# Kernel tuning notes

Hardware: AMD Instinct MI355X
Metric: run time of the kernel (lower is better)

## Reference

```python
import jax, jax.numpy as jnp
import numpy as np

BATCH = 2
L = 2048
D_MODEL = 1024
D_STATE = 16
D_CONV = 4
EXPAND = 2
D_INNER = EXPAND * D_MODEL  # 2048
DT_RANK = (D_MODEL + 15) // 16  # 64


def setup_inputs() -> dict:
    key = jax.random.key(0)
    ks = jax.random.split(key, 12)
    f = jnp.float32
    hidden_states = jax.random.normal(ks[0], (BATCH, L, D_MODEL), f)
    input2 = jax.random.normal(ks[1], (BATCH, L, D_MODEL), f)
    in_proj1_w = jax.random.normal(ks[2], (D_INNER, D_MODEL), f) * (D_MODEL ** -0.5)
    in_proj2_w = jax.random.normal(ks[3], (D_INNER, D_MODEL), f) * (D_MODEL ** -0.5)
    conv_w = jax.random.normal(ks[4], (D_INNER, 1, D_CONV), f) * (D_CONV ** -0.5)
    conv_b = jax.random.normal(ks[5], (D_INNER,), f) * 0.02
    x_proj_w = jax.random.normal(ks[6], (DT_RANK + 2 * D_STATE, D_INNER), f) * (D_INNER ** -0.5)
    dt_std = DT_RANK ** -0.5
    dt_proj_w = jax.random.uniform(ks[7], (D_INNER, DT_RANK), f, -dt_std, dt_std)
    # dt bias init: inverse softplus of log-uniform dt in [1e-3, 1e-1]
    dt = jnp.exp(jax.random.uniform(ks[8], (D_INNER,), f) * (np.log(0.1) - np.log(0.001)) + np.log(0.001))
    dt = jnp.clip(dt, 1e-4, None)
    dt_proj_b = dt + jnp.log(-jnp.expm1(-dt))
    # A_log init: log(1..d_state) broadcast over channels
    A_log = jnp.log(jnp.broadcast_to(jnp.arange(1, D_STATE + 1, dtype=f), (D_INNER, D_STATE)))
    D = jnp.ones((D_INNER,), f)
    out_proj_w = jax.random.normal(ks[9], (D_MODEL, D_INNER), f) * (D_INNER ** -0.5)
    return dict(hidden_states=hidden_states, input2=input2, in_proj1_w=in_proj1_w,
                in_proj2_w=in_proj2_w, conv_w=conv_w, conv_b=conv_b, x_proj_w=x_proj_w,
                dt_proj_w=dt_proj_w, dt_proj_b=dt_proj_b, A_log=A_log, D=D,
                out_proj_w=out_proj_w)


def _forward(hidden_states, input2, in_proj1_w, in_proj2_w, conv_w, conv_b,
             x_proj_w, dt_proj_w, dt_proj_b, A_log, D, out_proj_w):
    # in_proj: (B,L,Dm) -> (B,d_inner,L)
    x = jnp.einsum('bld,ed->bel', hidden_states, in_proj1_w)
    z = jnp.einsum('bld,ed->bel', input2, in_proj2_w)
    # causal depthwise conv1d (left pad d_conv-1, equiv to torch pad+truncate) + SiLU
    xc = jax.lax.conv_general_dilated(x, conv_w, (1,), [(D_CONV - 1, 0)],
                                      dimension_numbers=('NCH', 'OIH', 'NCH'),
                                      feature_group_count=D_INNER)
    x = jax.nn.silu(xc + conv_b[None, :, None])
    # x_proj -> dt, B, C
    x_dbl = jnp.einsum('bel,re->brl', x, x_proj_w)  # (B, dt_rank+2n, L)
    dt = x_dbl[:, :DT_RANK]
    Bm = x_dbl[:, DT_RANK:DT_RANK + D_STATE]       # (B, n, L)
    Cm = x_dbl[:, DT_RANK + D_STATE:]               # (B, n, L)
    delta = jnp.einsum('brl,er->bel', dt, dt_proj_w)
    delta = jax.nn.softplus(delta + dt_proj_b[None, :, None])  # (B, d_inner, L)
    A = -jnp.exp(A_log)  # (d_inner, n)
    # selective scan over time (time-major for lax.scan)
    dlt = jnp.transpose(delta, (2, 0, 1))  # (L, B, d)
    u = jnp.transpose(x, (2, 0, 1))        # (L, B, d)
    Bt = jnp.transpose(Bm, (2, 0, 1))      # (L, B, n)
    Ct = jnp.transpose(Cm, (2, 0, 1))      # (L, B, n)

    def step(state, inp):
        d_t, u_t, B_t, C_t = inp
        dA = jnp.exp(d_t[..., None] * A)                        # (B, d, n)
        state = state * dA + (d_t * u_t)[..., None] * B_t[:, None, :]
        y_t = jnp.einsum('bdn,bn->bd', state, C_t)
        return state, y_t

    init = jnp.zeros((hidden_states.shape[0], D_INNER, D_STATE), x.dtype)
    _, ys = jax.lax.scan(step, init, (dlt, u, Bt, Ct))
    y = jnp.transpose(ys, (1, 2, 0)) + D[None, :, None] * x  # (B, d, L)
    y = y * jax.nn.silu(z)
    out = jnp.einsum('bel,de->bld', y, out_proj_w)  # out_proj, no bias
    return out


def reference(hidden_states, input2, in_proj1_w, in_proj2_w, conv_w, conv_b,
              x_proj_w, dt_proj_w, dt_proj_b, A_log, D, out_proj_w):
    return _forward(hidden_states, input2, in_proj1_w, in_proj2_w, conv_w, conv_b,
                    x_proj_w, dt_proj_w, dt_proj_b, A_log, D, out_proj_w)
```

## Files before the change

kernel.cpp:

```cpp
#include <hip/hip_runtime.h>
#include <cstddef>
#include <cmath>
#include <type_traits>

#define BATCH 2
#define LSEQ 2048
#define DM 1024
#define DSTATE 16
#define DI 2048
#define DTR 64
#define XDR 96
#define NC 64
#define TC 32
#define PN (4096 * 96)

using f32x4 = __attribute__((ext_vector_type(4))) float;
using bf16x8 = __attribute__((ext_vector_type(8))) short;

__device__ __forceinline__ unsigned short f2bf(float f) {
  union { float f; unsigned int u; } c; c.f = f;
  unsigned int u = c.u;
  return (unsigned short)((u + 0x7FFFu + ((u >> 16) & 1u)) >> 16);
}
__device__ __forceinline__ float bf2f(unsigned short h) {
  union { unsigned int u; float f; } c; c.u = ((unsigned int)h) << 16;
  return c.f;
}
__device__ __forceinline__ unsigned int pack2(float a, float b) {
  return (unsigned int)f2bf(a) | ((unsigned int)f2bf(b) << 16);
}

__device__ __forceinline__ void gl_lds16(const void* g, void* l) {
  __builtin_amdgcn_global_load_lds(
      (const __attribute__((address_space(1))) void*)g,
      (__attribute__((address_space(3))) void*)l, 16, 0, 0);
}

__device__ __forceinline__ float softplus_fast(float x) {
  float ex = __expf(x);
  return (x > 20.f) ? x : __logf(1.f + ex);
}

__device__ __forceinline__ void pow_tree(float q1, float* dA) {
  float q2 = q1 * q1;
  float q3 = q2 * q1;
  float q4 = q2 * q2;
  float q8 = q4 * q4;
  float q5 = q4 * q1, q6 = q4 * q2, q7 = q4 * q3;
  dA[0] = q1;  dA[1] = q2;  dA[2] = q3;  dA[3] = q4;
  dA[4] = q5;  dA[5] = q6;  dA[6] = q7;  dA[7] = q8;
  dA[8] = q8 * q1;  dA[9] = q8 * q2;  dA[10] = q8 * q3;  dA[11] = q8 * q4;
  dA[12] = q8 * q5; dA[13] = q8 * q6; dA[14] = q8 * q7;  dA[15] = q8 * q8;
}

__global__ __launch_bounds__(256) void cvt_bf16_kernel(
    const float* __restrict__ s, unsigned short* __restrict__ d, int n8) {
  int i = blockIdx.x * 256 + threadIdx.x;
  if (i >= n8) return;
  const float4* sp = reinterpret_cast<const float4*>(s) + (size_t)i * 2;
  float4 a = sp[0], b = sp[1];
  uint4 v = make_uint4(pack2(a.x, a.y), pack2(a.z, a.w), pack2(b.x, b.y),
                       pack2(b.z, b.w));
  *(reinterpret_cast<uint4*>(d) + i) = v;
}

template <typename OutT>
__global__ __launch_bounds__(256) void gemm_bf16_t(
    const unsigned short* __restrict__ A, const unsigned short* __restrict__ B,
    OutT* __restrict__ C, int K, int lda, int ldb, int ldc) {
  __shared__ __align__(16) unsigned short As[128][64];
  __shared__ __align__(16) unsigned short Bs[128][64];

  const int tid = threadIdx.x;
  const int lane = tid & 63;
  const int w = tid >> 6;

  const int gx = gridDim.x;
  const int nwg = gx * gridDim.y;
  const int id = blockIdx.y * gx + blockIdx.x;
  const int cpx = nwg >> 3;
  const int lt = (id & 7) * cpx + (id >> 3);
  const size_t m0 = (size_t)(lt / gx) * 128;
  const size_t n0 = (size_t)(lt % gx) * 128;

  const int rsub = lane >> 3;
  const int sslot = (lane & 7) ^ rsub;
  const unsigned short* Ab = A + m0 * lda + (size_t)rsub * lda + sslot * 8;
  const unsigned short* Bb = B + n0 * ldb + (size_t)rsub * ldb + sslot * 8;

  f32x4 acc[4][4] = {};

  const int fr = lane & 15;
  const int q = lane >> 4;
  const int f7 = fr & 7;

  for (int k0 = 0; k0 < K; k0 += 64) {
#pragma unroll
    for (int i = 0; i < 4; ++i) {
      const int r0 = w * 32 + i * 8;
      gl_lds16(Ab + (size_t)r0 * lda + k0, &As[r0][0]);
      gl_lds16(Bb + (size_t)r0 * ldb + k0, &Bs[r0][0]);
    }
    __syncthreads();

    bf16x8 af[4][2], bf_[4][2];
#pragma unroll
    for (int i = 0; i < 4; ++i) {
#pragma unroll
      for (int kk = 0; kk < 2; ++kk) {
        const int sA = (((kk * 4 + q) ^ f7) << 3);
        af[i][kk] = *reinterpret_cast<const bf16x8*>(
            &As[(w >> 1) * 64 + i * 16 + fr][sA]);
        bf_[i][kk] = *reinterpret_cast<const bf16x8*>(
            &Bs[(w & 1) * 64 + i * 16 + fr][sA]);
      }
    }
#pragma unroll
    for (int kk = 0; kk < 2; ++kk)
#pragma unroll
      for (int i = 0; i < 4; ++i)
#pragma unroll
        for (int j = 0; j < 4; ++j)
          acc[i][j] = __builtin_amdgcn_mfma_f32_16x16x32_bf16(
              af[i][kk], bf_[j][kk], acc[i][j], 0, 0, 0);
    __syncthreads();
  }

  const int crb = q * 4;
#pragma unroll
  for (int i = 0; i < 4; ++i) {
    size_t row = m0 + (w >> 1) * 64 + i * 16 + crb;
#pragma unroll
    for (int j = 0; j < 4; ++j) {
      size_t col = n0 + (w & 1) * 64 + j * 16 + fr;
#pragma unroll
      for (int r = 0; r < 4; ++r) {
        if constexpr (std::is_same_v<OutT, unsigned short>)
          C[(row + r) * ldc + col] = f2bf(acc[i][j][r]);
        else
          C[(row + r) * ldc + col] = acc[i][j][r];
      }
    }
  }
}

__global__ __launch_bounds__(256) void gemm_delta(
    const unsigned short* __restrict__ A, const unsigned short* __restrict__ B,
    const float* __restrict__ bias, unsigned short* __restrict__ C, int K,
    int lda, int ldb, int ldc) {
  __shared__ __align__(16) unsigned short As[128][64];
  __shared__ __align__(16) unsigned short Bs[128][64];

  const int tid = threadIdx.x;
  const int lane = tid & 63;
  const int w = tid >> 6;

  const int gx = gridDim.x;
  const int nwg = gx * gridDim.y;
  const int id = blockIdx.y * gx + blockIdx.x;
  const int cpx = nwg >> 3;
  const int lt = (id & 7) * cpx + (id >> 3);
  const size_t m0 = (size_t)(lt / gx) * 128;
  const size_t n0 = (size_t)(lt % gx) * 128;

  const int rsub = lane >> 3;
  const int sslot = (lane & 7) ^ rsub;
  const unsigned short* Ab = A + m0 * lda + (size_t)rsub * lda + sslot * 8;
  const unsigned short* Bb = B + n0 * ldb + (size_t)rsub * ldb + sslot * 8;

  f32x4 acc[4][4] = {};

  const int fr = lane & 15;
  const int q = lane >> 4;
  const int f7 = fr & 7;

  for (int k0 = 0; k0 < K; k0 += 64) {
#pragma unroll
    for (int i = 0; i < 4; ++i) {
      const int r0 = w * 32 + i * 8;
      gl_lds16(Ab + (size_t)r0 * lda + k0, &As[r0][0]);
      gl_lds16(Bb + (size_t)r0 * ldb + k0, &Bs[r0][0]);
    }
    __syncthreads();

    bf16x8 af[4][2], bf_[4][2];
#pragma unroll
    for (int i = 0; i < 4; ++i) {
#pragma unroll
      for (int kk = 0; kk < 2; ++kk) {
        const int sA = (((kk * 4 + q) ^ f7) << 3);
        af[i][kk] = *reinterpret_cast<const bf16x8*>(
            &As[(w >> 1) * 64 + i * 16 + fr][sA]);
        bf_[i][kk] = *reinterpret_cast<const bf16x8*>(
            &Bs[(w & 1) * 64 + i * 16 + fr][sA]);
      }
    }
#pragma unroll
    for (int kk = 0; kk < 2; ++kk)
#pragma unroll
      for (int i = 0; i < 4; ++i)
#pragma unroll
        for (int j = 0; j < 4; ++j)
          acc[i][j] = __builtin_amdgcn_mfma_f32_16x16x32_bf16(
              af[i][kk], bf_[j][kk], acc[i][j], 0, 0, 0);
    __syncthreads();
  }

  const int crb = q * 4;
#pragma unroll
  for (int i = 0; i < 4; ++i) {
    size_t row = m0 + (w >> 1) * 64 + i * 16 + crb;
#pragma unroll
    for (int j = 0; j < 4; ++j) {
      size_t col = n0 + (w & 1) * 64 + j * 16 + fr;
      float bv = bias[col];
#pragma unroll
      for (int r = 0; r < 4; ++r)
        C[(row + r) * ldc + col] = f2bf(softplus_fast(acc[i][j][r] + bv));
    }
  }
}

__global__ __launch_bounds__(256) void gemm_xdbl(
    const unsigned short* __restrict__ A,
    const unsigned short* __restrict__ B,
    float* __restrict__ P) {
  __shared__ __align__(16) unsigned short As[128][64];
  __shared__ __align__(16) unsigned short Bs[96][64];

  const int tid = threadIdx.x;
  const int lane = tid & 63;
  const int w = tid >> 6;
  const size_t m0 = (size_t)blockIdx.x * 128;
  const int k0base = blockIdx.y * 512;

  const int rsub = lane >> 3;
  const int sslot = (lane & 7) ^ rsub;
  const unsigned short* Ab = A + m0 * DI + (size_t)rsub * DI + sslot * 8;
  const unsigned short* Bb = B + (size_t)rsub * DI + sslot * 8;

  f32x4 acc[4][3] = {};

  const int fr = lane & 15;
  const int q = lane >> 4;
  const int f7 = fr & 7;

  for (int ks = 0; ks < 8; ++ks) {
    const int k0 = k0base + ks * 64;
#pragma unroll
    for (int i = 0; i < 4; ++i) {
      const int r0 = w * 32 + i * 8;
      gl_lds16(Ab + (size_t)r0 * DI + k0, &As[r0][0]);
    }
#pragma unroll
    for (int i = 0; i < 3; ++i) {
      const int r0 = w * 24 + i * 8;
      gl_lds16(Bb + (size_t)r0 * DI + k0, &Bs[r0][0]);
    }
    __syncthreads();

    bf16x8 af[4][2], bf_[3][2];
#pragma unroll
    for (int kk = 0; kk < 2; ++kk) {
      const int sA = (((kk * 4 + q) ^ f7) << 3);
#pragma unroll
      for (int i = 0; i < 4; ++i)
        af[i][kk] = *reinterpret_cast<const bf16x8*>(
            &As[(w >> 1) * 64 + i * 16 + fr][sA]);
#pragma unroll
      for (int j = 0; j < 3; ++j)
        bf_[j][kk] = *reinterpret_cast<const bf16x8*>(
            &Bs[(w & 1) * 48 + j * 16 + fr][sA]);
    }
#pragma unroll
    for (int kk = 0; kk < 2; ++kk)
#pragma unroll
      for (int i = 0; i < 4; ++i)
#pragma unroll
        for (int j = 0; j < 3; ++j)
          acc[i][j] = __builtin_amdgcn_mfma_f32_16x16x32_bf16(
              af[i][kk], bf_[j][kk], acc[i][j], 0, 0, 0);
    __syncthreads();
  }

  float* Pz = P + (size_t)blockIdx.y * PN;
  const int crb = q * 4;
#pragma unroll
  for (int i = 0; i < 4; ++i) {
    size_t row = m0 + (w >> 1) * 64 + i * 16 + crb;
#pragma unroll
    for (int j = 0; j < 3; ++j) {
      int col = (w & 1) * 48 + j * 16 + fr;
#pragma unroll
      for (int r = 0; r < 4; ++r) Pz[(row + r) * XDR + col] = acc[i][j][r];
    }
  }
}

__global__ __launch_bounds__(256) void reduce4x_kernel(
    const float* __restrict__ P, unsigned short* __restrict__ dtB,
    float* __restrict__ BC) {
  int i = blockIdx.x * 256 + threadIdx.x;
  int row = i / XDR, col = i - row * XDR;
  float s = (P[i] + P[PN + i]) + (P[2 * PN + i] + P[3 * PN + i]);
  if (col < 64)
    dtB[row * 64 + col] = f2bf(s);
  else
    BC[row * 32 + (col - 64)] = s;
}

__global__ __launch_bounds__(256) void conv_silu_kernel(
    const float* __restrict__ x, const float* __restrict__ w,
    const float* __restrict__ cb, unsigned short* __restrict__ out) {
  int idx = blockIdx.x * 256 + threadIdx.x;
  int e4 = idx % (DI / 4);
  int bl = idx / (DI / 4);
  int l = bl % LSEQ;
  int e = e4 * 4;

  const float4* cw = reinterpret_cast<const float4*>(w);
  float4 w0 = cw[e], w1 = cw[e + 1], w2 = cw[e + 2], w3 = cw[e + 3];
  float4 acc = *reinterpret_cast<const float4*>(&cb[e]);

#define TAPK(K, COMP)                                                       \
  {                                                                         \
    int ls = l - 3 + (K);                                                   \
    if (ls >= 0) {                                                          \
      float4 xv = *reinterpret_cast<const float4*>(                         \
          &x[((size_t)(bl) - 3 + (K)) * DI + e]);                           \
      acc.x = fmaf(xv.x, w0.COMP, acc.x);                                   \
      acc.y = fmaf(xv.y, w1.COMP, acc.y);                                   \
      acc.z = fmaf(xv.z, w2.COMP, acc.z);                                   \
      acc.w = fmaf(xv.w, w3.COMP, acc.w);                                   \
    }                                                                       \
  }
  TAPK(0, x)
  TAPK(1, y)
  TAPK(2, z)
  TAPK(3, w)
#undef TAPK

  acc.x = acc.x / (1.f + expf(-acc.x));
  acc.y = acc.y / (1.f + expf(-acc.y));
  acc.z = acc.z / (1.f + expf(-acc.z));
  acc.w = acc.w / (1.f + expf(-acc.w));
  *reinterpret_cast<uint2*>(&out[(size_t)bl * DI + e]) =
      make_uint2(pack2(acc.x, acc.y), pack2(acc.z, acc.w));
}

__global__ __launch_bounds__(256) void scan_passA(
    const unsigned short* __restrict__ dB, const unsigned short* __restrict__ u,
    const float* __restrict__ bc, const float* __restrict__ A_log,
    float* __restrict__ sEnd, float* __restrict__ sProd) {
  int g = blockIdx.x * 256 + threadIdx.x;
  int e = g & (DI - 1);
  int c = (g >> 11) & (NC - 1);
  int b = g >> 17;

  const float nA0 = -__expf(A_log[e * DSTATE]);
  bool aok = true;
#pragma unroll
  for (int n = 1; n < DSTATE; ++n) {
    float nAn = -__expf(A_log[e * DSTATE + n]);
    aok = aok && (fabsf(nAn - (float)(n + 1) * nA0) <= 1e-4f * fabsf(nAn));
  }

  size_t off = ((size_t)b * LSEQ + c * TC) * DI + e;
  size_t boff = ((size_t)b * LSEQ + c * TC) * 32;

  float s[DSTATE], P[DSTATE];
#pragma unroll
  for (int n = 0; n < DSTATE; ++n) { s[n] = 0.f; P[n] = 1.f; }

  float d = bf2f(dB[off]);
  float ut = bf2f(u[off]);

  for (int t = 0; t < TC; ++t) {
    float d_n = 0.f, ut_n = 0.f;
    if (t + 1 < TC) {
      d_n = bf2f(dB[off + DI]);
      ut_n = bf2f(u[off + DI]);
    }

    float db = d * ut;
    float dA[DSTATE];
    if (aok) {
      pow_tree(__expf(d * nA0), dA);
    } else {
#pragma unroll
      for (int n = 0; n < DSTATE; ++n)
        dA[n] = __expf(-d * __expf(A_log[e * DSTATE + n]));
    }
    const float4* bcp = reinterpret_cast<const float4*>(&bc[boff]);
    float4 B0 = bcp[0], B1 = bcp[1], B2 = bcp[2], B3 = bcp[3];
    float Bv[DSTATE] = {B0.x, B0.y, B0.z, B0.w, B1.x, B1.y, B1.z, B1.w,
                        B2.x, B2.y, B2.z, B2.w, B3.x, B3.y, B3.z, B3.w};
#pragma unroll
    for (int n = 0; n < DSTATE; ++n) {
      s[n] = fmaf(s[n], dA[n], db * Bv[n]);
      P[n] *= dA[n];
    }
    off += DI;
    boff += 32;
    d = d_n; ut = ut_n;
  }

  size_t o = (((size_t)b * NC + c) * DI + e) * DSTATE;
  float4* se = reinterpret_cast<float4*>(&sEnd[o]);
  float4* sp = reinterpret_cast<float4*>(&sProd[o]);
  se[0] = make_float4(s[0], s[1], s[2], s[3]);
  se[1] = make_float4(s[4], s[5], s[6], s[7]);
  se[2] = make_float4(s[8], s[9], s[10], s[11]);
  se[3] = make_float4(s[12], s[13], s[14], s[15]);
  sp[0] = make_float4(P[0], P[1], P[2], P[3]);
  sp[1] = make_float4(P[4], P[5], P[6], P[7]);
  sp[2] = make_float4(P[8], P[9], P[10], P[11]);
  sp[3] = make_float4(P[12], P[13], P[14], P[15]);
}

__global__ __launch_bounds__(256) void scan_passB(
    float* __restrict__ sEnd, const float* __restrict__ sProd) {
  int g = blockIdx.x * 256 + threadIdx.x;
  int n = g & 15;
  int e = (g >> 4) & (DI - 1);
  int b = g >> 15;
  float s = 0.f;
  for (int c = 0; c < NC; ++c) {
    size_t o = (((size_t)b * NC + c) * DI + e) * DSTATE + n;
    float se = sEnd[o];
    float sp = sProd[o];
    sEnd[o] = s;
    s = fmaf(s, sp, se);
  }
}

__global__ __launch_bounds__(256) void scan_passC(
    const unsigned short* __restrict__ dB, const unsigned short* __restrict__ u,
    const unsigned short* __restrict__ z, const float* __restrict__ bc,
    const float* __restrict__ A_log, const float* __restrict__ Dv,
    const float* __restrict__ sInit, unsigned short* __restrict__ gOut) {
  int g = blockIdx.x * 256 + threadIdx.x;
  int e = g & (DI - 1);
  int c = (g >> 11) & (NC - 1);
  int b = g >> 17;

  const float nA0 = -__expf(A_log[e * DSTATE]);
  bool aok = true;
#pragma unroll
  for (int n = 1; n < DSTATE; ++n) {
    float nAn = -__expf(A_log[e * DSTATE + n]);
    aok = aok && (fabsf(nAn - (float)(n + 1) * nA0) <= 1e-4f * fabsf(nAn));
  }
  const float Dval = Dv[e];

  size_t off = ((size_t)b * LSEQ + c * TC) * DI + e;
  size_t boff = ((size_t)b * LSEQ + c * TC) * 32;

  float s[DSTATE];
  {
    size_t o = (((size_t)b * NC + c) * DI + e) * DSTATE;
    const float4* si = reinterpret_cast<const float4*>(&sInit[o]);
    float4 s0 = si[0], s1 = si[1], s2 = si[2], s3 = si[3];
    s[0] = s0.x; s[1] = s0.y; s[2] = s0.z; s[3] = s0.w;
    s[4] = s1.x; s[5] = s1.y; s[6] = s1.z; s[7] = s1.w;
    s[8] = s2.x; s[9] = s2.y; s[10] = s2.z; s[11] = s2.w;
    s[12] = s3.x; s[13] = s3.y; s[14] = s3.z; s[15] = s3.w;
  }

  float d = bf2f(dB[off]);
  float ut = bf2f(u[off]);
  float zt = bf2f(z[off]);

  for (int t = 0; t < TC; ++t) {
    float d_n = 0.f, ut_n = 0.f, zt_n = 0.f;
    if (t + 1 < TC) {
      d_n = bf2f(dB[off + DI]);
      ut_n = bf2f(u[off + DI]);
      zt_n = bf2f(z[off + DI]);
    }

    float db = d * ut;
    float dA[DSTATE];
    if (aok) {
      pow_tree(__expf(d * nA0), dA);
    } else {
#pragma unroll
      for (int n = 0; n < DSTATE; ++n)
        dA[n] = __expf(-d * __expf(A_log[e * DSTATE + n]));
    }
    const float4* bcp = reinterpret_cast<const float4*>(&bc[boff]);
    float4 B0 = bcp[0], B1 = bcp[1], B2 = bcp[2], B3 = bcp[3];
    float4 C0 = bcp[4], C1 = bcp[5], C2 = bcp[6], C3 = bcp[7];
    float Bv[DSTATE] = {B0.x, B0.y, B0.z, B0.w, B1.x, B1.y, B1.z, B1.w,
                        B2.x, B2.y, B2.z, B2.w, B3.x, B3.y, B3.z, B3.w};
    float Cv[DSTATE] = {C0.x, C0.y, C0.z, C0.w, C1.x, C1.y, C1.z, C1.w,
                        C2.x, C2.y, C2.z, C2.w, C3.x, C3.y, C3.z, C3.w};
    float y0 = 0.f, y1 = 0.f, y2 = 0.f, y3 = 0.f;
#pragma unroll
    for (int n = 0; n < 4; ++n) {
      s[n] = fmaf(s[n], dA[n], db * Bv[n]);
      y0 = fmaf(s[n], Cv[n], y0);
      s[n + 4] = fmaf(s[n + 4], dA[n + 4], db * Bv[n + 4]);
      y1 = fmaf(s[n + 4], Cv[n + 4], y1);
      s[n + 8] = fmaf(s[n + 8], dA[n + 8], db * Bv[n + 8]);
      y2 = fmaf(s[n + 8], Cv[n + 8], y2);
      s[n + 12] = fmaf(s[n + 12], dA[n + 12], db * Bv[n + 12]);
      y3 = fmaf(s[n + 12], Cv[n + 12], y3);
    }
    float y = (y0 + y1) + (y2 + y3);
    float gate = zt / (1.f + __expf(-zt));
    gOut[off] = f2bf((y + Dval * ut) * gate);

    off += DI;
    boff += 32;
    d = d_n; ut = ut_n; zt = zt_n;
  }
}

extern "C" void kernel_launch(void* const* d_in, const int* in_sizes, int n_in,
                              void* d_out, int out_size, void* d_ws,
                              size_t ws_size, hipStream_t stream) {
  const float* hs = (const float*)d_in[0];
  const float* in2 = (const float*)d_in[1];
  const float* w1 = (const float*)d_in[2];
  const float* w2 = (const float*)d_in[3];
  const float* cw = (const float*)d_in[4];
  const float* cb = (const float*)d_in[5];
  const float* xpw = (const float*)d_in[6];
  const float* dtw = (const float*)d_in[7];
  const float* dtb = (const float*)d_in[8];
  const float* alog = (const float*)d_in[9];
  const float* Dv = (const float*)d_in[10];
  const float* ow = (const float*)d_in[11];
  float* out = (float*)d_out;

  const size_t BLE = (size_t)BATCH * LSEQ * DI;
  const size_t BLM = (size_t)BATCH * LSEQ * DM;
  const size_t WN = (size_t)DI * DM;
  const size_t SC = (size_t)BATCH * NC * DI * DSTATE;

  float* W = (float*)d_ws;
  float* bufX = W;
  float* M2 = W + BLE;
  float* M3 = M2 + BLE / 2;
  float* M4 = M3 + BLE / 2;
  float* sEnd = M4 + BLE / 2;
  float* sProd = sEnd + SC;
  float* BC = sProd + SC;

  unsigned short* hsb = (unsigned short*)M2;
  unsigned short* zb = (unsigned short*)M2;
  unsigned short* in2b = (unsigned short*)M3;
  unsigned short* ub = (unsigned short*)M3;
  unsigned short* wb1 = (unsigned short*)M4;
  unsigned short* wb2 = wb1 + WN;
  float* xdblP = M4;
  unsigned short* xpwB = (unsigned short*)(M4 + 4 * PN);
  unsigned short* dtB = (unsigned short*)(M4 + 4 * PN + 98304 + 16);
  unsigned short* dtwB = (unsigned short*)(M4 + 4 * PN + 98304 + 131072 + 32);
  unsigned short* bufG = (unsigned short*)M4;
  unsigned short* dB = (unsigned short*)bufX;
  unsigned short* owb = (unsigned short*)sProd;

  const int M = BATCH * LSEQ;
  dim3 blk(256);

  cvt_bf16_kernel<<<(int)(BLM / 8 / 256), blk, 0, stream>>>(hs, hsb,
                                                            (int)(BLM / 8));
  cvt_bf16_kernel<<<(int)(BLM / 8 / 256), blk, 0, stream>>>(in2, in2b,
                                                            (int)(BLM / 8));
  cvt_bf16_kernel<<<(int)(WN / 8 / 256), blk, 0, stream>>>(w1, wb1,
                                                           (int)(WN / 8));
  cvt_bf16_kernel<<<(int)(WN / 8 / 256), blk, 0, stream>>>(w2, wb2,
                                                           (int)(WN / 8));
  gemm_bf16_t<float><<<dim3(DI / 128, M / 128), blk, 0, stream>>>(
      hsb, wb1, bufX, DM, DM, DM, DI);
  gemm_bf16_t<unsigned short><<<dim3(DI / 128, M / 128), blk, 0, stream>>>(
      in2b, wb2, zb, DM, DM, DM, DI);
  conv_silu_kernel<<<(M * (DI / 4)) / 256, blk, 0, stream>>>(bufX, cw, cb, ub);
  cvt_bf16_kernel<<<96, blk, 0, stream>>>(xpw, xpwB, XDR * DI / 8);
  cvt_bf16_kernel<<<64, blk, 0, stream>>>(dtw, dtwB, DI * DTR / 8);
  gemm_xdbl<<<dim3(M / 128, 4), blk, 0, stream>>>(ub, xpwB, xdblP);
  reduce4x_kernel<<<(M * XDR) / 256, blk, 0, stream>>>(xdblP, dtB, BC);
  gemm_delta<<<dim3(DI / 128, M / 128), blk, 0, stream>>>(
      dtB, dtwB, dtb, dB, DTR, DTR, DTR, DI);
  scan_passA<<<(BATCH * DI * NC) / 256, blk, 0, stream>>>(dB, ub, BC, alog,
                                                          sEnd, sProd);
  scan_passB<<<(BATCH * DI * DSTATE) / 256, blk, 0, stream>>>(sEnd, sProd);
  cvt_bf16_kernel<<<(int)(WN / 8 / 256), blk, 0, stream>>>(ow, owb,
                                                           (int)(WN / 8));
  scan_passC<<<(BATCH * DI * NC) / 256, blk, 0, stream>>>(
      dB, ub, zb, BC, alog, Dv, sEnd, bufG);
  gemm_bf16_t<float><<<dim3(DM / 128, M / 128), blk, 0, stream>>>(
      bufG, owb, out, DI, DI, DI, DM);
}
```

Baseline: 247.0 us.

## Store x projection in bf16, merge conversion launches, deepen scan prefetch

```diff
diff --git a/kernel.cpp b/kernel.cpp
--- a/kernel.cpp
+++ b/kernel.cpp
@@ -64,6 +64,26 @@
   *(reinterpret_cast<uint4*>(d) + i) = v;
 }
 
+__global__ __launch_bounds__(256) void cvt2_bf16_kernel(
+    const float* __restrict__ s1, unsigned short* __restrict__ d1,
+    const float* __restrict__ s2, unsigned short* __restrict__ d2, int n8) {
+  int i = blockIdx.x * 256 + threadIdx.x;
+  const float* s;
+  unsigned short* d;
+  int k;
+  if (i < n8) {
+    s = s1; d = d1; k = i;
+  } else {
+    s = s2; d = d2; k = i - n8;
+    if (k >= n8) return;
+  }
+  const float4* sp = reinterpret_cast<const float4*>(s) + (size_t)k * 2;
+  float4 a = sp[0], b = sp[1];
+  uint4 v = make_uint4(pack2(a.x, a.y), pack2(a.z, a.w), pack2(b.x, b.y),
+                       pack2(b.z, b.w));
+  *(reinterpret_cast<uint4*>(d) + k) = v;
+}
+
 template <typename OutT>
 __global__ __launch_bounds__(256) void gemm_bf16_t(
     const unsigned short* __restrict__ A, const unsigned short* __restrict__ B,
@@ -310,7 +330,7 @@
 }
 
 __global__ __launch_bounds__(256) void conv_silu_kernel(
-    const float* __restrict__ x, const float* __restrict__ w,
+    const unsigned short* __restrict__ x, const float* __restrict__ w,
     const float* __restrict__ cb, unsigned short* __restrict__ out) {
   int idx = blockIdx.x * 256 + threadIdx.x;
   int e4 = idx % (DI / 4);
@@ -326,12 +346,12 @@
   {                                                                         \
     int ls = l - 3 + (K);                                                   \
     if (ls >= 0) {                                                          \
-      float4 xv = *reinterpret_cast<const float4*>(                         \
+      uint2 xv = *reinterpret_cast<const uint2*>(                           \
           &x[((size_t)(bl) - 3 + (K)) * DI + e]);                           \
-      acc.x = fmaf(xv.x, w0.COMP, acc.x);                                   \
-      acc.y = fmaf(xv.y, w1.COMP, acc.y);                                   \
-      acc.z = fmaf(xv.z, w2.COMP, acc.z);                                   \
-      acc.w = fmaf(xv.w, w3.COMP, acc.w);                                   \
+      acc.x = fmaf(bf2f((unsigned short)(xv.x & 0xffff)), w0.COMP, acc.x);  \
+      acc.y = fmaf(bf2f((unsigned short)(xv.x >> 16)), w1.COMP, acc.y);     \
+      acc.z = fmaf(bf2f((unsigned short)(xv.y & 0xffff)), w2.COMP, acc.z);  \
+      acc.w = fmaf(bf2f((unsigned short)(xv.y >> 16)), w3.COMP, acc.w);     \
     }                                                                       \
   }
   TAPK(0, x)
@@ -365,44 +385,52 @@
     aok = aok && (fabsf(nAn - (float)(n + 1) * nA0) <= 1e-4f * fabsf(nAn));
   }
 
-  size_t off = ((size_t)b * LSEQ + c * TC) * DI + e;
-  size_t boff = ((size_t)b * LSEQ + c * TC) * 32;
+  const size_t off = ((size_t)b * LSEQ + c * TC) * DI + e;
+  const size_t boff0 = ((size_t)b * LSEQ + c * TC) * 32;
 
   float s[DSTATE], P[DSTATE];
 #pragma unroll
   for (int n = 0; n < DSTATE; ++n) { s[n] = 0.f; P[n] = 1.f; }
 
-  float d = bf2f(dB[off]);
-  float ut = bf2f(u[off]);
-
-  for (int t = 0; t < TC; ++t) {
-    float d_n = 0.f, ut_n = 0.f;
-    if (t + 1 < TC) {
-      d_n = bf2f(dB[off + DI]);
-      ut_n = bf2f(u[off + DI]);
-    }
-
-    float db = d * ut;
-    float dA[DSTATE];
-    if (aok) {
-      pow_tree(__expf(d * nA0), dA);
-    } else {
-#pragma unroll
-      for (int n = 0; n < DSTATE; ++n)
-        dA[n] = __expf(-d * __expf(A_log[e * DSTATE + n]));
-    }
-    const float4* bcp = reinterpret_cast<const float4*>(&bc[boff]);
-    float4 B0 = bcp[0], B1 = bcp[1], B2 = bcp[2], B3 = bcp[3];
-    float Bv[DSTATE] = {B0.x, B0.y, B0.z, B0.w, B1.x, B1.y, B1.z, B1.w,
-                        B2.x, B2.y, B2.z, B2.w, B3.x, B3.y, B3.z, B3.w};
-#pragma unroll
-    for (int n = 0; n < DSTATE; ++n) {
-      s[n] = fmaf(s[n], dA[n], db * Bv[n]);
-      P[n] *= dA[n];
-    }
-    off += DI;
-    boff += 32;
-    d = d_n; ut = ut_n;
+  unsigned short dq[4], uq[4];
+#pragma unroll
+  for (int j = 0; j < 4; ++j) {
+    size_t o = off + (size_t)j * DI;
+    dq[j] = dB[o];
+    uq[j] = u[o];
+  }
+
+  for (int tb = 0; tb < TC; tb += 4) {
+#pragma unroll
+    for (int j = 0; j < 4; ++j) {
+      const int t = tb + j;
+      float d = bf2f(dq[j]);
+      float ut = bf2f(uq[j]);
+      if (t + 4 < TC) {
+        size_t o = off + (size_t)(t + 4) * DI;
+        dq[j] = dB[o];
+        uq[j] = u[o];
+      }
+      float db = d * ut;
+      float dA[DSTATE];
+      if (aok) {
+        pow_tree(__expf(d * nA0), dA);
+      } else {
+#pragma unroll
+        for (int n = 0; n < DSTATE; ++n)
+          dA[n] = __expf(-d * __expf(A_log[e * DSTATE + n]));
+      }
+      const float4* bcp =
+          reinterpret_cast<const float4*>(&bc[boff0 + (size_t)t * 32]);
+      float4 B0 = bcp[0], B1 = bcp[1], B2 = bcp[2], B3 = bcp[3];
+      float Bv[DSTATE] = {B0.x, B0.y, B0.z, B0.w, B1.x, B1.y, B1.z, B1.w,
+                          B2.x, B2.y, B2.z, B2.w, B3.x, B3.y, B3.z, B3.w};
+#pragma unroll
+      for (int n = 0; n < DSTATE; ++n) {
+        s[n] = fmaf(s[n], dA[n], db * Bv[n]);
+        P[n] *= dA[n];
+      }
+    }
   }
 
   size_t o = (((size_t)b * NC + c) * DI + e) * DSTATE;
@@ -453,8 +481,8 @@
   }
   const float Dval = Dv[e];
 
-  size_t off = ((size_t)b * LSEQ + c * TC) * DI + e;
-  size_t boff = ((size_t)b * LSEQ + c * TC) * 32;
+  const size_t off = ((size_t)b * LSEQ + c * TC) * DI + e;
+  const size_t boff0 = ((size_t)b * LSEQ + c * TC) * 32;
 
   float s[DSTATE];
   {
@@ -467,53 +495,61 @@
     s[12] = s3.x; s[13] = s3.y; s[14] = s3.z; s[15] = s3.w;
   }
 
-  float d = bf2f(dB[off]);
-  float ut = bf2f(u[off]);
-  float zt = bf2f(z[off]);
-
-  for (int t = 0; t < TC; ++t) {
-    float d_n = 0.f, ut_n = 0.f, zt_n = 0.f;
-    if (t + 1 < TC) {
-      d_n = bf2f(dB[off + DI]);
-      ut_n = bf2f(u[off + DI]);
-      zt_n = bf2f(z[off + DI]);
-    }
-
-    float db = d * ut;
-    float dA[DSTATE];
-    if (aok) {
-      pow_tree(__expf(d * nA0), dA);
-    } else {
-#pragma unroll
-      for (int n = 0; n < DSTATE; ++n)
-        dA[n] = __expf(-d * __expf(A_log[e * DSTATE + n]));
-    }
-    const float4* bcp = reinterpret_cast<const float4*>(&bc[boff]);
-    float4 B0 = bcp[0], B1 = bcp[1], B2 = bcp[2], B3 = bcp[3];
-    float4 C0 = bcp[4], C1 = bcp[5], C2 = bcp[6], C3 = bcp[7];
-    float Bv[DSTATE] = {B0.x, B0.y, B0.z, B0.w, B1.x, B1.y, B1.z, B1.w,
-                        B2.x, B2.y, B2.z, B2.w, B3.x, B3.y, B3.z, B3.w};
-    float Cv[DSTATE] = {C0.x, C0.y, C0.z, C0.w, C1.x, C1.y, C1.z, C1.w,
-                        C2.x, C2.y, C2.z, C2.w, C3.x, C3.y, C3.z, C3.w};
-    float y0 = 0.f, y1 = 0.f, y2 = 0.f, y3 = 0.f;
-#pragma unroll
-    for (int n = 0; n < 4; ++n) {
-      s[n] = fmaf(s[n], dA[n], db * Bv[n]);
-      y0 = fmaf(s[n], Cv[n], y0);
-      s[n + 4] = fmaf(s[n + 4], dA[n + 4], db * Bv[n + 4]);
-      y1 = fmaf(s[n + 4], Cv[n + 4], y1);
-      s[n + 8] = fmaf(s[n + 8], dA[n + 8], db * Bv[n + 8]);
-      y2 = fmaf(s[n + 8], Cv[n + 8], y2);
-      s[n + 12] = fmaf(s[n + 12], dA[n + 12], db * Bv[n + 12]);
-      y3 = fmaf(s[n + 12], Cv[n + 12], y3);
-    }
-    float y = (y0 + y1) + (y2 + y3);
-    float gate = zt / (1.f + __expf(-zt));
-    gOut[off] = f2bf((y + Dval * ut) * gate);
-
-    off += DI;
-    boff += 32;
-    d = d_n; ut = ut_n; zt = zt_n;
+  unsigned short dq[4], uq[4], zq[4];
+#pragma unroll
+  for (int j = 0; j < 4; ++j) {
+    size_t o = off + (size_t)j * DI;
+    dq[j] = dB[o];
+    uq[j] = u[o];
+    zq[j] = z[o];
+  }
+
+  for (int tb = 0; tb < TC; tb += 4) {
+#pragma unroll
+    for (int j = 0; j < 4; ++j) {
+      const int t = tb + j;
+      float d = bf2f(dq[j]);
+      float ut = bf2f(uq[j]);
+      float zt = bf2f(zq[j]);
+      if (t + 4 < TC) {
+        size_t o = off + (size_t)(t + 4) * DI;
+        dq[j] = dB[o];
+        uq[j] = u[o];
+        zq[j] = z[o];
+      }
+      float db = d * ut;
+      float dA[DSTATE];
+      if (aok) {
+        pow_tree(__expf(d * nA0), dA);
+      } else {
+#pragma unroll
+        for (int n = 0; n < DSTATE; ++n)
+          dA[n] = __expf(-d * __expf(A_log[e * DSTATE + n]));
+      }
+      const float4* bcp =
+          reinterpret_cast<const float4*>(&bc[boff0 + (size_t)t * 32]);
+      float4 B0 = bcp[0], B1 = bcp[1], B2 = bcp[2], B3 = bcp[3];
+      float4 C0 = bcp[4], C1 = bcp[5], C2 = bcp[6], C3 = bcp[7];
+      float Bv[DSTATE] = {B0.x, B0.y, B0.z, B0.w, B1.x, B1.y, B1.z, B1.w,
+                          B2.x, B2.y, B2.z, B2.w, B3.x, B3.y, B3.z, B3.w};
+      float Cv[DSTATE] = {C0.x, C0.y, C0.z, C0.w, C1.x, C1.y, C1.z, C1.w,
+                          C2.x, C2.y, C2.z, C2.w, C3.x, C3.y, C3.z, C3.w};
+      float y0 = 0.f, y1 = 0.f, y2 = 0.f, y3 = 0.f;
+#pragma unroll
+      for (int n = 0; n < 4; ++n) {
+        s[n] = fmaf(s[n], dA[n], db * Bv[n]);
+        y0 = fmaf(s[n], Cv[n], y0);
+        s[n + 4] = fmaf(s[n + 4], dA[n + 4], db * Bv[n + 4]);
+        y1 = fmaf(s[n + 4], Cv[n + 4], y1);
+        s[n + 8] = fmaf(s[n + 8], dA[n + 8], db * Bv[n + 8]);
+        y2 = fmaf(s[n + 8], Cv[n + 8], y2);
+        s[n + 12] = fmaf(s[n + 12], dA[n + 12], db * Bv[n + 12]);
+        y3 = fmaf(s[n + 12], Cv[n + 12], y3);
+      }
+      float y = (y0 + y1) + (y2 + y3);
+      float gate = zt / (1.f + __expf(-zt));
+      gOut[off + (size_t)t * DI] = f2bf((y + Dval * ut) * gate);
+    }
   }
 }
 
@@ -559,25 +595,23 @@
   unsigned short* dtB = (unsigned short*)(M4 + 4 * PN + 98304 + 16);
   unsigned short* dtwB = (unsigned short*)(M4 + 4 * PN + 98304 + 131072 + 32);
   unsigned short* bufG = (unsigned short*)M4;
+  unsigned short* xpreB = (unsigned short*)bufX;
   unsigned short* dB = (unsigned short*)bufX;
   unsigned short* owb = (unsigned short*)sProd;
 
   const int M = BATCH * LSEQ;
   dim3 blk(256);
 
-  cvt_bf16_kernel<<<(int)(BLM / 8 / 256), blk, 0, stream>>>(hs, hsb,
-                                                            (int)(BLM / 8));
-  cvt_bf16_kernel<<<(int)(BLM / 8 / 256), blk, 0, stream>>>(in2, in2b,
-                                                            (int)(BLM / 8));
-  cvt_bf16_kernel<<<(int)(WN / 8 / 256), blk, 0, stream>>>(w1, wb1,
-                                                           (int)(WN / 8));
-  cvt_bf16_kernel<<<(int)(WN / 8 / 256), blk, 0, stream>>>(w2, wb2,
-                                                           (int)(WN / 8));
-  gemm_bf16_t<float><<<dim3(DI / 128, M / 128), blk, 0, stream>>>(
-      hsb, wb1, bufX, DM, DM, DM, DI);
+  cvt2_bf16_kernel<<<(int)(2 * (BLM / 8) / 256), blk, 0, stream>>>(
+      hs, hsb, in2, in2b, (int)(BLM / 8));
+  cvt2_bf16_kernel<<<(int)(2 * (WN / 8) / 256), blk, 0, stream>>>(
+      w1, wb1, w2, wb2, (int)(WN / 8));
+  gemm_bf16_t<unsigned short><<<dim3(DI / 128, M / 128), blk, 0, stream>>>(
+      hsb, wb1, xpreB, DM, DM, DM, DI);
   gemm_bf16_t<unsigned short><<<dim3(DI / 128, M / 128), blk, 0, stream>>>(
       in2b, wb2, zb, DM, DM, DM, DI);
-  conv_silu_kernel<<<(M * (DI / 4)) / 256, blk, 0, stream>>>(bufX, cw, cb, ub);
+  conv_silu_kernel<<<(M * (DI / 4)) / 256, blk, 0, stream>>>(xpreB, cw, cb,
+                                                             ub);
   cvt_bf16_kernel<<<96, blk, 0, stream>>>(xpw, xpwB, XDR * DI / 8);
   cvt_bf16_kernel<<<64, blk, 0, stream>>>(dtw, dtwB, DI * DTR / 8);
   gemm_xdbl<<<dim3(M / 128, 4), blk, 0, stream>>>(ub, xpwB, xdblP);
```

Result: slower. 265.1 us (+7.3%).
